# Optimization experiments

Hardware: AMD Instinct MI355X
Metric: run time of the kernel (lower is better)

Reference implementation:

```python
import jax, jax.numpy as jnp
import numpy as np

V, E, H = 50000, 256, 256   # vocab, emb_dim, hid_dim
R, S, W = 64, 32, 64        # reviews, sentences/review, words/sentence
UF = 20                     # user feature dim


def _bigru_last(x, wih, whh, bih, bhh):
    """Bidirectional GRU over x [B,T,D]; returns sum of final hidden states of
    the two directions, shape [B,H]. Params stacked over direction axis 0."""
    Hh = whh.shape[-1]

    def onedir(xd, wi, wh, bi, bh):
        gx = jnp.einsum('btd,gd->btg', xd, wi) + bi  # [B,T,3H] input gates precomputed

        def step(h, gxt):
            gh = h @ wh.T + bh
            r = jax.nn.sigmoid(gxt[:, :Hh] + gh[:, :Hh])
            z = jax.nn.sigmoid(gxt[:, Hh:2 * Hh] + gh[:, Hh:2 * Hh])
            n = jnp.tanh(gxt[:, 2 * Hh:] + r * gh[:, 2 * Hh:])
            return (1.0 - z) * n + z * h, None

        h0 = jnp.zeros((xd.shape[0], Hh), xd.dtype)
        hT, _ = jax.lax.scan(step, h0, jnp.swapaxes(gx, 0, 1))
        return hT

    return (onedir(x, wih[0], whh[0], bih[0], bhh[0])
            + onedir(x[:, ::-1], wih[1], whh[1], bih[1], bhh[1]))


def setup_inputs() -> dict:
    key = jax.random.key(0)
    ks = iter(jax.random.split(key, 40))

    def wmat(shape, scale=0.05):
        return jax.random.normal(next(ks), shape, jnp.float32) * scale

    inp = {}
    inp['inputs'] = jax.random.randint(next(ks), (R, S, W), 0, V)
    inp['sent_lengths'] = jax.random.randint(next(ks), (R, S), 1, W)
    inp['sent_counts'] = jax.random.randint(next(ks), (R,), 1, S)
    inp['user_feats'] = jax.random.normal(next(ks), (R, UF), jnp.float32)
    inp['embed'] = wmat((V, E))
    for name, din in (('wg', E), ('sg', H), ('rg', H + UF)):
        inp[name + '_wih'] = wmat((2, 3 * H, din))
        inp[name + '_whh'] = wmat((2, 3 * H, H))
        inp[name + '_bih'] = jnp.zeros((2, 3 * H), jnp.float32)
        inp[name + '_bhh'] = jnp.zeros((2, 3 * H), jnp.float32)
    inp['rfc_w1'] = wmat((H // 2, H + UF)); inp['rfc_b1'] = jnp.zeros((H // 2,), jnp.float32)
    inp['rfc_w2'] = wmat((1, H // 2));      inp['rfc_b2'] = jnp.zeros((1,), jnp.float32)
    inp['pfc_w1'] = wmat((H // 2, H));      inp['pfc_b1'] = jnp.zeros((H // 2,), jnp.float32)
    inp['pfc_w2'] = wmat((9, H // 2));      inp['pfc_b2'] = jnp.zeros((9,), jnp.float32)
    inp['uf_w'] = jnp.ones((UF,), jnp.float32)  # user_feats_weights
    return inp


def reference(inputs, sent_lengths, sent_counts, user_feats, embed,
              wg_wih, wg_whh, wg_bih, wg_bhh,
              sg_wih, sg_whh, sg_bih, sg_bhh,
              rg_wih, rg_whh, rg_bih, rg_bhh,
              rfc_w1, rfc_b1, rfc_w2, rfc_b2,
              pfc_w1, pfc_b1, pfc_w2, pfc_b2, uf_w):
    Rr, Sr, Wr = inputs.shape
    emb = embed[inputs]  # [R,S,W,E]  (dropout = identity in eval mode)
    # word-level bi-GRU, all R*S sentences batched together
    sent = _bigru_last(emb.reshape(Rr * Sr, Wr, emb.shape[-1]),
                       wg_wih, wg_whh, wg_bih, wg_bhh).reshape(Rr, Sr, -1)
    # sentence-level bi-GRU, batch over reviews
    rev = _bigru_last(sent, sg_wih, sg_whh, sg_bih, sg_bhh)  # [R,H]
    # F.normalize(user_feats) * user_feats_weights
    nrm = jnp.maximum(jnp.linalg.norm(user_feats, axis=-1, keepdims=True), 1e-12)
    p_batch = jnp.concatenate([rev, (user_feats / nrm) * uf_w], axis=-1)  # [R,H+20]
    r_stars = (jax.nn.selu(p_batch @ rfc_w1.T + rfc_b1) @ rfc_w2.T + rfc_b2)[:, 0]  # [R]
    # review-level bi-GRU over the sequence of reviews (batch 1)
    doc = _bigru_last(p_batch[None], rg_wih, rg_whh, rg_bih, rg_bhh)[0]  # [H]
    p_stars = jax.nn.selu(doc @ pfc_w1.T + pfc_b1) @ pfc_w2.T + pfc_b2  # [9]
    return p_stars, r_stars
```

## Files before the change

### kernel.cpp

```cpp
#include <hip/hip_runtime.h>
#include <math.h>

#define R_ 64
#define S_ 32
#define W_ 64
#define H_ 256
#define UF_ 20
#define TC 4

typedef short bf16x8 __attribute__((ext_vector_type(8)));
typedef float f32x4  __attribute__((ext_vector_type(4)));

#define MFMA(a,b,c) __builtin_amdgcn_mfma_f32_16x16x32_bf16((a),(b),(c),0,0,0)

typedef const unsigned int __attribute__((address_space(1)))* gp_t;
typedef unsigned int __attribute__((address_space(3)))* lp_t;
#define GLOAD16(SRC, DST) \
  __builtin_amdgcn_global_load_lds((gp_t)(const void*)(SRC), (lp_t)(void*)(DST), 16, 0, 0)

#define BFRAG(ff) ((ff) < 40 ? Breg[(ff) < 40 ? (ff) : 0] \
                 : *(const bf16x8*)&Bl[w][(ff) >= 40 ? (ff)-40 : 0][l*8])

__device__ __forceinline__ float sigf(float x){ return 1.0f/(1.0f+__expf(-x)); }
__device__ __forceinline__ float tanhf_(float x){ float e=__expf(2.0f*x); return 1.0f-2.0f/(e+1.0f); }
__device__ __forceinline__ float seluf_(float x){
  const float sc=1.0507009873554805f, al=1.6732632423543772f;
  return x>0.0f ? sc*x : sc*al*(expf(x)-1.0f);
}
__device__ __forceinline__ short tobf(float f){
  unsigned u=__float_as_uint(f); u += 0x7fffu + ((u>>16)&1u); return (short)(u>>16);
}
__device__ __forceinline__ float bf2f(short s){
  return __uint_as_float(((unsigned)(unsigned short)s) << 16);
}
__device__ __forceinline__ unsigned pk2(float a, float b){
  return (unsigned)(unsigned short)tobf(a) | ((unsigned)(unsigned short)tobf(b) << 16);
}

__global__ void prep_word_w(const float* __restrict__ wih, const float* __restrict__ whh,
                            short* __restrict__ Bw)
{
  int idx = blockIdx.x*256 + threadIdx.x;
  int lane = idx & 63;
  int rest = idx >> 6;
  int f  = rest % 6;  rest /= 6;
  int kt = rest % 16; rest /= 16;
  int w  = rest % 8;
  int d  = rest / 8;
  int gate = f >> 1;
  int j = 32*w + (f&1)*16 + (lane&15);
  int row = gate*256 + j;
  const float* W = (kt < 8 ? wih : whh) + (size_t)d*768*256;
  int k = (kt&7)*32 + (lane>>4)*8;
  short* dst = Bw + ((((size_t)(d*8 + w)*16 + kt)*6 + f)*64 + lane)*8;
#pragma unroll
  for (int jj=0;jj<8;jj++) dst[jj] = tobf(W[(size_t)row*256 + k + jj]);
}

__global__ void prep_rnn_w(const float* __restrict__ whh, short* __restrict__ Bs)
{
  int idx = blockIdx.x*256 + threadIdx.x;
  int lane = idx & 63;
  int rest = idx >> 6;
  int f  = rest % 6; rest /= 6;
  int kt = rest % 8; rest /= 8;
  int w  = rest % 8;
  int d  = rest / 8;
  int j = 32*w + (f&1)*16 + (lane&15);
  int row = (f>>1)*256 + j;
  const float* W = whh + (size_t)d*768*256;
  int k = kt*32 + (lane>>4)*8;
  short* dst = Bs + ((((size_t)(d*8 + w)*8 + kt)*6 + f)*64 + lane)*8;
#pragma unroll
  for (int jj=0;jj<8;jj++) dst[jj] = tobf(W[(size_t)row*256 + k + jj]);
}

__global__ void prep_gemm_w(const float* __restrict__ Wsrc, short* __restrict__ Bg)
{
  int idx = blockIdx.x*256 + threadIdx.x;
  int lane = idx & 63;
  int rest = idx >> 6;
  int kt = rest % 8;
  int nt = rest / 8;
  int n = nt*16 + (lane&15);
  int k = kt*32 + (lane>>4)*8;
  short* dst = Bg + (((size_t)nt*8 + kt)*64 + lane)*8;
#pragma unroll
  for (int jj=0;jj<8;jj++) dst[jj] = tobf(Wsrc[(size_t)n*256 + k + jj]);
}

__global__ __launch_bounds__(256) void gemm_gxu(
    const short* __restrict__ Ab, const float* __restrict__ Af,
    const int* __restrict__ toks, const short* __restrict__ Bg,
    short* __restrict__ C, long Czoff,
    int mode, int t0, int Mclamp, int Cstride)
{
  const int z  = blockIdx.z;
  const int m0 = blockIdx.x * 64;
  const int yt = blockIdx.y * 8;
  const int ntb = (mode == 2 ? z*48 : 0) + yt;
  const int tid = threadIdx.x;
  const int w = tid >> 6, l = tid & 63;
  const int c = l & 15, q = l >> 4;
  __shared__ short As[64][264];
  {
    const int row = tid >> 2, c0 = (tid & 3) * 64;
    if (mode == 0) {
      const uint4* s = (const uint4*)(Ab + (size_t)(m0+row)*256 + c0);
#pragma unroll
      for (int i = 0; i < 8; i++) *(uint4*)&As[row][c0 + i*8] = s[i];
    } else {
      int r;
      if (mode == 1) {
        r = m0 + row; if (r >= Mclamp) r = Mclamp - 1;
      } else {
        const int rr = m0 + row;
        const int s_ = rr / TC, i_ = rr % TC;
        const int wd = z ? (63 - (t0 + i_)) : (t0 + i_);
        r = toks[s_*64 + wd];
      }
      const float* s = Af + (size_t)r*256 + c0;
#pragma unroll
      for (int i = 0; i < 8; i++) {
        float4 v0 = *(const float4*)(s + i*8);
        float4 v1 = *(const float4*)(s + i*8 + 4);
        uint4 u;
        u.x = pk2(v0.x, v0.y); u.y = pk2(v0.z, v0.w);
        u.z = pk2(v1.x, v1.y); u.w = pk2(v1.z, v1.w);
        *(uint4*)&As[row][c0 + i*8] = u;
      }
    }
  }
  __syncthreads();
  f32x4 acc[4][2];
#pragma unroll
  for (int a = 0; a < 4; a++) { acc[a][0] = (f32x4)0.f; acc[a][1] = (f32x4)0.f; }
#pragma unroll
  for (int kt = 0; kt < 8; kt++) {
    const int ko = kt*32 + q*8;
    bf16x8 a0 = *(const bf16x8*)&As[ 0+c][ko];
    bf16x8 a1 = *(const bf16x8*)&As[16+c][ko];
    bf16x8 a2 = *(const bf16x8*)&As[32+c][ko];
    bf16x8 a3 = *(const bf16x8*)&As[48+c][ko];
    bf16x8 b0 = *(const bf16x8*)&Bg[(((size_t)(ntb + 2*w    )*8 + kt)*64 + l)*8];
    bf16x8 b1 = *(const bf16x8*)&Bg[(((size_t)(ntb + 2*w + 1)*8 + kt)*64 + l)*8];
    acc[0][0]=MFMA(a0,b0,acc[0][0]); acc[1][0]=MFMA(a1,b0,acc[1][0]);
    acc[2][0]=MFMA(a2,b0,acc[2][0]); acc[3][0]=MFMA(a3,b0,acc[3][0]);
    acc[0][1]=MFMA(a0,b1,acc[0][1]); acc[1][1]=MFMA(a1,b1,acc[1][1]);
    acc[2][1]=MFMA(a2,b1,acc[2][1]); acc[3][1]=MFMA(a3,b1,acc[3][1]);
  }
  short* Cz = C + (size_t)z * Czoff;
#pragma unroll
  for (int mt = 0; mt < 4; mt++)
#pragma unroll
  for (int nt = 0; nt < 2; nt++)
#pragma unroll
  for (int rg = 0; rg < 4; rg++)
    Cz[(size_t)(m0 + mt*16 + q*4 + rg)*Cstride + (yt + 2*w + nt)*16 + c] =
        tobf(acc[mt][nt][rg]);
}

__device__ __forceinline__ void stage_issue(
    short* dstbase,
    int mode, int d, int g, int w, int l,
    int nwords, int t0, int tt,
    const int* tokp, const short* gxF, const short* gxB)
{
  const char* bF = (const char*)gxF;
  const char* bB = (const char*)gxB;
#pragma unroll
  for (int i = 0; i < 3; i++) {
    const int off = i*1024 + l*16;
    const int rl  = (off >= 1536) ? 1 : 0;
    const int col = off - rl*1536;
    const char* src;
    if (mode == 0) {
      const int tx  = d ? (nwords - 1 - tt) : tt;
      const int tok = tokp[(2*w + rl)*64 + tx];
      src = bF + (size_t)tok*3072 + d*1536 + col;
    } else if (mode == 1) {
      const int ri = (g*16 + 2*w + rl)*TC + (tt - t0);
      src = (d ? bB : bF) + (size_t)ri*1536 + col;
    } else {
      const int se  = d ? (nwords - 1 - tt) : tt;
      const int row = g*16 + 2*w + rl;
      src = bF + ((size_t)row*nwords + se)*3072 + (size_t)d*1536 + col;
    }
    GLOAD16(src, dstbase + (size_t)w*1536 + i*512);
  }
}

__global__ __launch_bounds__(512, 2) void gru_rec(
    const int* __restrict__ toks,
    const short* __restrict__ gxF, const short* __restrict__ gxB,
    const short* __restrict__ Bh, int wstride, int koff,
    const float* __restrict__ bih, const float* __restrict__ bhh,
    float* __restrict__ hstate, int NS,
    int t0, int nsteps, int mode, int nwords)
{
  const int d = blockIdx.x & 1;
  const int g = blockIdx.x >> 1;
  const int tid = threadIdx.x;
  const int w = tid >> 6, l = tid & 63;
  const int c = l & 15, q = l >> 4;

  __shared__ short gbuf[2][16][768];
  __shared__ short hbf[2][16][264];
  __shared__ short Bl[8][8][512];
  __shared__ int   tokL[1024];

  if (mode == 0)
    for (int i = tid; i < 1024; i += 512) tokL[i] = toks[(size_t)g*1024 + i];

  bf16x8 Breg[40];
  {
    const short* Bb = Bh + (size_t)(d*8 + w)*wstride + (size_t)koff*3072 + l*8;
#pragma unroll
    for (int ff = 0; ff < 48; ff++) {
      bf16x8 v = *(const bf16x8*)(Bb + ff*512);
      if (ff < 40) Breg[ff] = v;
      else *(bf16x8*)&Bl[w][ff-40][l*8] = v;
    }
  }

  float bR[2], bZ[2], bNX[2], bNH[2];
#pragma unroll
  for (int jt = 0; jt < 2; jt++) {
    int j = 32*w + jt*16 + c;
    bR[jt]  = bih[d*768 + j]       + bhh[d*768 + j];
    bZ[jt]  = bih[d*768 + 256 + j] + bhh[d*768 + 256 + j];
    bNX[jt] = bih[d*768 + 512 + j];
    bNH[jt] = bhh[d*768 + 512 + j];
  }

  float hst[2][4];
  const int cur0 = t0 & 1;
  if (t0 == 0) {
#pragma unroll
    for (int a = 0; a < 2; a++)
#pragma unroll
    for (int r = 0; r < 4; r++) hst[a][r] = 0.0f;
  } else {
#pragma unroll
    for (int jt = 0; jt < 2; jt++)
#pragma unroll
    for (int rg = 0; rg < 4; rg++)
      hst[jt][rg] = hstate[((size_t)d*NS + g*16 + q*4 + rg)*256 + 32*w + jt*16 + c];
  }
#pragma unroll
  for (int jt = 0; jt < 2; jt++)
#pragma unroll
  for (int rg = 0; rg < 4; rg++)
    hbf[cur0][q*4 + rg][32*w + jt*16 + c] = tobf(hst[jt][rg]);

  stage_issue((short*)gbuf[cur0], mode, d, g, w, l, nwords, t0, t0,
              (mode == 0) ? toks + (size_t)g*1024 : (const int*)nullptr, gxF, gxB);

  __syncthreads();

  const int tend = t0 + nsteps;
  for (int t = t0; t < tend; t++) {
    const int cur = t & 1, nxt = 1 - cur;

    if (t + 1 < tend)
      stage_issue((short*)gbuf[nxt], mode, d, g, w, l, nwords, t0, t + 1,
                  tokL, gxF, gxB);

    f32x4 accR[2], accZ[2], accNH[2];
#pragma unroll
    for (int a = 0; a < 2; a++) { accR[a]=(f32x4)0.f; accZ[a]=(f32x4)0.f; accNH[a]=(f32x4)0.f; }
#pragma unroll
    for (int kt = 0; kt < 8; kt++) {
      bf16x8 a0 = *(const bf16x8*)&hbf[cur][c][kt*32 + q*8];
      bf16x8 b0 = BFRAG(kt*6+0), b1 = BFRAG(kt*6+1), b2 = BFRAG(kt*6+2),
             b3 = BFRAG(kt*6+3), b4 = BFRAG(kt*6+4), b5 = BFRAG(kt*6+5);
      accR[0]=MFMA(a0,b0,accR[0]);  accR[1]=MFMA(a0,b1,accR[1]);
      accZ[0]=MFMA(a0,b2,accZ[0]);  accZ[1]=MFMA(a0,b3,accZ[1]);
      accNH[0]=MFMA(a0,b4,accNH[0]); accNH[1]=MFMA(a0,b5,accNH[1]);
    }

#pragma unroll
    for (int jt = 0; jt < 2; jt++)
#pragma unroll
    for (int rg = 0; rg < 4; rg++) {
      const int m = q*4 + rg;
      const int j = 32*w + jt*16 + c;
      const float gr = bf2f(gbuf[cur][m][j]);
      const float gz = bf2f(gbuf[cur][m][256 + j]);
      const float gn = bf2f(gbuf[cur][m][512 + j]);
      const float r = sigf(gr + bR[jt] + accR[jt][rg]);
      const float z = sigf(gz + bZ[jt] + accZ[jt][rg]);
      const float n = tanhf_(gn + bNX[jt] + r*(accNH[jt][rg] + bNH[jt]));
      float h = hst[jt][rg];
      h = (1.0f - z)*n + z*h;
      hst[jt][rg] = h;
      hbf[nxt][m][j] = tobf(h);
    }
    __syncthreads();
  }

#pragma unroll
  for (int jt = 0; jt < 2; jt++)
#pragma unroll
  for (int rg = 0; rg < 4; rg++)
    hstate[((size_t)d*NS + g*16 + q*4 + rg)*256 + 32*w + jt*16 + c] = hst[jt][rg];
}

__global__ void add2bf(const float* __restrict__ a, const float* __restrict__ b,
                       short* __restrict__ o)
{
  int i = (blockIdx.x*256 + threadIdx.x)*4;
  float4 x = *(const float4*)&a[i];
  float4 y = *(const float4*)&b[i];
  *(uint2*)&o[i] = make_uint2(pk2(x.x+y.x, x.y+y.y), pk2(x.z+y.z, x.w+y.w));
}

__global__ __launch_bounds__(512, 2) void rev_gru(
    const float* __restrict__ gx, const short* __restrict__ Br,
    const float* __restrict__ bih, const float* __restrict__ bhh,
    float* __restrict__ doc)
{
  const int d = blockIdx.x;
  const int tid = threadIdx.x;
  const int w = tid >> 6, l = tid & 63;
  const int c = l & 15, q = l >> 4;

  __shared__ short hbf[2][16][264];
  __shared__ short Bl[8][8][512];
  for (int i = tid; i < 16*264; i += 512) ((short*)hbf[0])[i] = 0;

  bf16x8 Breg[40];
  {
    const short* Bbase = Br + (size_t)(d*8 + w)*8*6*512 + l*8;
#pragma unroll
    for (int ff = 0; ff < 48; ff++) {
      bf16x8 v = *(const bf16x8*)(Bbase + ff*512);
      if (ff < 40) Breg[ff] = v;
      else *(bf16x8*)&Bl[w][ff-40][l*8] = v;
    }
  }

  float bR[2], bZ[2], bNX[2], bNH[2];
#pragma unroll
  for (int jt = 0; jt < 2; jt++) {
    int j = 32*w + jt*16 + c;
    bR[jt]  = bih[d*768 + j]       + bhh[d*768 + j];
    bZ[jt]  = bih[d*768 + 256 + j] + bhh[d*768 + 256 + j];
    bNX[jt] = bih[d*768 + 512 + j];
    bNH[jt] = bhh[d*768 + 512 + j];
  }
  float hst[2][4];
#pragma unroll
  for (int a=0;a<2;a++)
#pragma unroll
  for (int r=0;r<4;r++) hst[a][r] = 0.0f;
  __syncthreads();

  for (int t = 0; t < 64; t++) {
    const int cur = t & 1, nxt = 1 - cur;
    const int teff = (d == 0) ? t : (63 - t);
    float gr[2], gz[2], gn[2];
#pragma unroll
    for (int jt = 0; jt < 2; jt++) {
      const int j = 32*w + jt*16 + c;
      const size_t row = (size_t)teff*1536 + d*768;
      gr[jt] = gx[row + j]; gz[jt] = gx[row + 256 + j]; gn[jt] = gx[row + 512 + j];
    }
    f32x4 accR[2], accZ[2], accNH[2];
#pragma unroll
    for (int a=0;a<2;a++) { accR[a]=(f32x4)0.f; accZ[a]=(f32x4)0.f; accNH[a]=(f32x4)0.f; }
#pragma unroll
    for (int kt = 0; kt < 8; kt++) {
      bf16x8 a0 = *(const bf16x8*)&hbf[cur][c][kt*32 + q*8];
      bf16x8 b0 = BFRAG(kt*6+0), b1 = BFRAG(kt*6+1), b2 = BFRAG(kt*6+2),
             b3 = BFRAG(kt*6+3), b4 = BFRAG(kt*6+4), b5 = BFRAG(kt*6+5);
      accR[0]=MFMA(a0,b0,accR[0]);  accR[1]=MFMA(a0,b1,accR[1]);
      accZ[0]=MFMA(a0,b2,accZ[0]);  accZ[1]=MFMA(a0,b3,accZ[1]);
      accNH[0]=MFMA(a0,b4,accNH[0]); accNH[1]=MFMA(a0,b5,accNH[1]);
    }
#pragma unroll
    for (int jt = 0; jt < 2; jt++)
#pragma unroll
    for (int rg = 0; rg < 4; rg++) {
      const float r = sigf(gr[jt] + bR[jt] + accR[jt][rg]);
      const float z = sigf(gz[jt] + bZ[jt] + accZ[jt][rg]);
      const float n = tanhf_(gn[jt] + bNX[jt] + r*(accNH[jt][rg] + bNH[jt]));
      float h = hst[jt][rg];
      h = (1.0f - z)*n + z*h;
      hst[jt][rg] = h;
      hbf[nxt][q*4 + rg][32*w + jt*16 + c] = tobf(h);
    }
    __syncthreads();
  }
  if (q == 0) {
#pragma unroll
    for (int jt = 0; jt < 2; jt++)
      doc[d*256 + 32*w + jt*16 + c] = hst[jt][0];
  }
}

__global__ __launch_bounds__(256) void gemm_nt16(
    const float* __restrict__ A, const float* __restrict__ B, float* __restrict__ C,
    int M, int N, int K)
{
  const int m0 = blockIdx.x * 16;
  const int n0 = blockIdx.y * 64;
  const int tid = threadIdx.x;
  __shared__ float As[16][17];
  __shared__ float Bs[16][68];
  float acc[4] = {0,0,0,0};
  const int m  = tid >> 4, n4 = (tid & 15) * 4;
  const int bn = tid >> 2, bk = (tid & 3) * 4;
  for (int k0 = 0; k0 < K; k0 += 16) {
    const int ak = tid & 15;
    float av = (k0 + ak < K) ? A[(size_t)(m0+m)*K + k0 + ak] : 0.0f;
    float4 b4 = make_float4(0,0,0,0);
    if (k0 + bk < K) b4 = *(const float4*)&B[(size_t)(n0+bn)*K + k0 + bk];
    __syncthreads();
    As[ak][m] = av;
    Bs[bk+0][bn]=b4.x; Bs[bk+1][bn]=b4.y; Bs[bk+2][bn]=b4.z; Bs[bk+3][bn]=b4.w;
    __syncthreads();
#pragma unroll
    for (int k = 0; k < 16; k++) {
      const float a = As[k][m];
      const float4 bb = *(const float4*)&Bs[k][n4];
      acc[0]+=a*bb.x; acc[1]+=a*bb.y; acc[2]+=a*bb.z; acc[3]+=a*bb.w;
    }
  }
  *(float4*)&C[(size_t)(m0+m)*N + n0+n4] = make_float4(acc[0],acc[1],acc[2],acc[3]);
}

__global__ void pbatch_k(const float* __restrict__ hs, const float* __restrict__ uf,
                         const float* __restrict__ ufw, float* __restrict__ pb)
{
  const int r = blockIdx.x, tid = threadIdx.x;
  __shared__ float nrm;
  if (tid == 0) {
    float s = 0.f;
    for (int i = 0; i < UF_; i++) { const float v = uf[r*UF_ + i]; s += v*v; }
    nrm = fmaxf(sqrtf(s), 1e-12f);
  }
  __syncthreads();
  if (tid < H_)  pb[r*276 + tid] = hs[r*H_ + tid] + hs[(size_t)R_*H_ + r*H_ + tid];
  if (tid < UF_) pb[r*276 + H_ + tid] = uf[r*UF_ + tid] / nrm * ufw[tid];
}

__global__ void rstars_k(const float* __restrict__ pb,
                         const float* __restrict__ w1, const float* __restrict__ b1,
                         const float* __restrict__ w2, const float* __restrict__ b2,
                         float* __restrict__ out)
{
  const int r = blockIdx.x, tid = threadIdx.x;
  __shared__ float ps[276];
  __shared__ float s1[128];
  for (int i = tid; i < 276; i += 128) ps[i] = pb[r*276 + i];
  __syncthreads();
  float a = b1[tid];
  for (int k = 0; k < 276; k++) a += ps[k] * w1[tid*276 + k];
  s1[tid] = seluf_(a);
  __syncthreads();
  if (tid == 0) {
    float s = b2[0];
    for (int k = 0; k < 128; k++) s += s1[k] * w2[k];
    out[9 + r] = s;
  }
}

__global__ void pstars_k(const float* __restrict__ doc2,
                         const float* __restrict__ w1, const float* __restrict__ b1,
                         const float* __restrict__ w2, const float* __restrict__ b2,
                         float* __restrict__ out)
{
  const int tid = threadIdx.x;
  __shared__ float dc[256];
  __shared__ float s1[128];
  dc[tid]       = doc2[tid]       + doc2[256 + tid];
  dc[128 + tid] = doc2[128 + tid] + doc2[384 + tid];
  __syncthreads();
  float a = b1[tid];
  for (int k = 0; k < 256; k++) a += dc[k] * w1[tid*256 + k];
  s1[tid] = seluf_(a);
  __syncthreads();
  if (tid < 9) {
    float s = b2[tid];
    for (int k = 0; k < 128; k++) s += s1[k] * w2[tid*128 + k];
    out[tid] = s;
  }
}

extern "C" void kernel_launch(void* const* d_in, const int* in_sizes, int n_in,
                              void* d_out, int out_size, void* d_ws, size_t ws_size,
                              hipStream_t stream)
{
  const int*   toks   = (const int*)  d_in[0];
  const float* uf     = (const float*)d_in[3];
  const float* embed  = (const float*)d_in[4];
  const float* wg_wih = (const float*)d_in[5];
  const float* wg_whh = (const float*)d_in[6];
  const float* wg_bih = (const float*)d_in[7];
  const float* wg_bhh = (const float*)d_in[8];
  const float* sg_wih = (const float*)d_in[9];
  const float* sg_whh = (const float*)d_in[10];
  const float* sg_bih = (const float*)d_in[11];
  const float* sg_bhh = (const float*)d_in[12];
  const float* rg_wih = (const float*)d_in[13];
  const float* rg_whh = (const float*)d_in[14];
  const float* rg_bih = (const float*)d_in[15];
  const float* rg_bhh = (const float*)d_in[16];
  const float* rfc_w1 = (const float*)d_in[17];
  const float* rfc_b1 = (const float*)d_in[18];
  const float* rfc_w2 = (const float*)d_in[19];
  const float* rfc_b2 = (const float*)d_in[20];
  const float* pfc_w1 = (const float*)d_in[21];
  const float* pfc_b1 = (const float*)d_in[22];
  const float* pfc_w2 = (const float*)d_in[23];
  const float* pfc_b2 = (const float*)d_in[24];
  const float* uf_w   = (const float*)d_in[25];
  float* out = (float*)d_out;
  float* ws  = (float*)d_ws;
  (void)in_sizes; (void)n_in; (void)out_size;

  const size_t OFF_BW   = 0;
  const size_t OFF_BS   = OFF_BW  + 393216;
  const size_t OFF_BR   = OFF_BS  + 196608;
  const size_t OFF_BG   = OFF_BR  + 196608;
  const size_t OFF_BGW  = OFF_BG  + 196608;
  const size_t OFF_HF   = OFF_BGW + 196608;
  const size_t OFF_SB   = OFF_HF  + 1048576;
  const size_t OFF_GXS  = OFF_SB  + 262144;
  const size_t OFF_HS   = OFF_GXS + 1572864;
  const size_t OFF_PB   = OFF_HS  + 32768;
  const size_t OFF_GXR  = OFF_PB  + 17664;
  const size_t OFF_DOC  = OFF_GXR + 98304;
  const size_t OFF_GXT  = OFF_DOC + 512;
  const size_t TOT_A    = OFF_GXT + (size_t)50048*1536/2;

  short* Bw   = (short*)(ws + OFF_BW);
  short* Bs   = (short*)(ws + OFF_BS);
  short* Br   = (short*)(ws + OFF_BR);
  short* Bg   = (short*)(ws + OFF_BG);
  short* Bgw  = (short*)(ws + OFF_BGW);
  float* hfin = ws + OFF_HF;
  short* sentb= (short*)(ws + OFF_SB);
  short* gxs  = (short*)(ws + OFF_GXS);
  float* hs   = ws + OFF_HS;
  float* pb   = ws + OFF_PB;
  float* gxr  = ws + OFF_GXR;
  float* doc  = ws + OFF_DOC;
  short* gxf  = (short*)(ws + OFF_GXT);
  short* gxb  = gxf + (size_t)8192*768;
  short* gxv  = (short*)(ws + OFF_GXT);

  const bool big = ws_size >= TOT_A * sizeof(float);

  prep_word_w<<<384, 256, 0, stream>>>(wg_wih, wg_whh, Bw);
  prep_rnn_w<<<192, 256, 0, stream>>>(sg_whh, Bs);
  prep_rnn_w<<<192, 256, 0, stream>>>(rg_whh, Br);
  prep_gemm_w<<<192, 256, 0, stream>>>(sg_wih, Bg);
  prep_gemm_w<<<192, 256, 0, stream>>>(wg_wih, Bgw);

  if (big) {
    gemm_gxu<<<dim3(782, 12, 1), 256, 0, stream>>>(
        nullptr, embed, nullptr, Bgw, gxv, 0, 1, 0, 50000, 1536);
    gru_rec<<<256, 512, 0, stream>>>(toks, gxv, nullptr, Bw, 49152, 8,
        wg_bih, wg_bhh, hfin, 2048, 0, 64, 0, 64);
  } else {
    for (int tc = 0; tc < 64/TC; tc++) {
      gemm_gxu<<<dim3(128, 6, 2), 256, 0, stream>>>(
          nullptr, embed, toks, Bgw, gxf, (long)8192*768, 2, tc*TC, 0, 768);
      gru_rec<<<256, 512, 0, stream>>>(toks, gxf, gxb, Bw, 49152, 8,
          wg_bih, wg_bhh, hfin, 2048, tc*TC, TC, 1, 64);
    }
  }
  add2bf<<<512, 256, 0, stream>>>(hfin, hfin + (size_t)2048*256, sentb);

  gemm_gxu<<<dim3(32, 12, 1), 256, 0, stream>>>(
      sentb, nullptr, nullptr, Bg, gxs, 0, 0, 0, 2048, 1536);
  gru_rec<<<8, 512, 0, stream>>>(nullptr, gxs, nullptr, Bs, 24576, 0,
      sg_bih, sg_bhh, hs, 64, 0, 32, 2, 32);

  pbatch_k<<<R_, 256, 0, stream>>>(hs, uf, uf_w, pb);
  rstars_k<<<R_, 128, 0, stream>>>(pb, rfc_w1, rfc_b1, rfc_w2, rfc_b2, out);

  gemm_nt16<<<dim3(4, 24), 256, 0, stream>>>(pb, rg_wih, gxr, 64, 1536, 276);
  rev_gru<<<2, 512, 0, stream>>>(gxr, Br, rg_bih, rg_bhh, doc);
  pstars_k<<<1, 128, 0, stream>>>(doc, pfc_w1, pfc_b1, pfc_w2, pfc_b2, out);
}
```

Measured before the change: 783.9 us.

## Fold GRU biases into input GEMMs and load gate inputs directly into registers

The r/z biases (bih+bhh) and the n input bias are now added in the input-projection GEMM epilogues, so the recurrent kernels only keep the hidden n bias. The async global-to-LDS double-buffered staging of gate inputs is removed. Each lane instead gathers its own gate values straight into registers every step, and the h buffer uses an XOR swizzle in place of padding to avoid LDS bank conflicts. rev_gru only updates row 0 since batch is 1, and the doc sum moves to a separate kernel. Per-step direct global gathers may expose latency that the earlier prefetch hid.

```diff
diff --git a/kernel.cpp b/kernel.cpp
--- a/kernel.cpp
+++ b/kernel.cpp
@@ -12,11 +12,6 @@
 typedef float f32x4  __attribute__((ext_vector_type(4)));
 
 #define MFMA(a,b,c) __builtin_amdgcn_mfma_f32_16x16x32_bf16((a),(b),(c),0,0,0)
-
-typedef const unsigned int __attribute__((address_space(1)))* gp_t;
-typedef unsigned int __attribute__((address_space(3)))* lp_t;
-#define GLOAD16(SRC, DST) \
-  __builtin_amdgcn_global_load_lds((gp_t)(const void*)(SRC), (lp_t)(void*)(DST), 16, 0, 0)
 
 #define BFRAG(ff) ((ff) < 40 ? Breg[(ff) < 40 ? (ff) : 0] \
                  : *(const bf16x8*)&Bl[w][(ff) >= 40 ? (ff)-40 : 0][l*8])
@@ -92,6 +87,7 @@
 __global__ __launch_bounds__(256) void gemm_gxu(
     const short* __restrict__ Ab, const float* __restrict__ Af,
     const int* __restrict__ toks, const short* __restrict__ Bg,
+    const float* __restrict__ bih, const float* __restrict__ bhh,
     short* __restrict__ C, long Czoff,
     int mode, int t0, int Mclamp, int Cstride)
 {
@@ -131,6 +127,13 @@
       }
     }
   }
+  float bias[2];
+#pragma unroll
+  for (int nt = 0; nt < 2; nt++) {
+    const int coln = (yt + 2*w + nt)*16 + c;
+    const int bidx = (mode == 2 ? z*768 : 0) + coln;
+    bias[nt] = bih[bidx] + ((bidx % 768) < 512 ? bhh[bidx] : 0.0f);
+  }
   __syncthreads();
   f32x4 acc[4][2];
 #pragma unroll
@@ -157,44 +160,14 @@
 #pragma unroll
   for (int rg = 0; rg < 4; rg++)
     Cz[(size_t)(m0 + mt*16 + q*4 + rg)*Cstride + (yt + 2*w + nt)*16 + c] =
-        tobf(acc[mt][nt][rg]);
-}
-
-__device__ __forceinline__ void stage_issue(
-    short* dstbase,
-    int mode, int d, int g, int w, int l,
-    int nwords, int t0, int tt,
-    const int* tokp, const short* gxF, const short* gxB)
-{
-  const char* bF = (const char*)gxF;
-  const char* bB = (const char*)gxB;
-#pragma unroll
-  for (int i = 0; i < 3; i++) {
-    const int off = i*1024 + l*16;
-    const int rl  = (off >= 1536) ? 1 : 0;
-    const int col = off - rl*1536;
-    const char* src;
-    if (mode == 0) {
-      const int tx  = d ? (nwords - 1 - tt) : tt;
-      const int tok = tokp[(2*w + rl)*64 + tx];
-      src = bF + (size_t)tok*3072 + d*1536 + col;
-    } else if (mode == 1) {
-      const int ri = (g*16 + 2*w + rl)*TC + (tt - t0);
-      src = (d ? bB : bF) + (size_t)ri*1536 + col;
-    } else {
-      const int se  = d ? (nwords - 1 - tt) : tt;
-      const int row = g*16 + 2*w + rl;
-      src = bF + ((size_t)row*nwords + se)*3072 + (size_t)d*1536 + col;
-    }
-    GLOAD16(src, dstbase + (size_t)w*1536 + i*512);
-  }
+        tobf(acc[mt][nt][rg] + bias[nt]);
 }
 
 __global__ __launch_bounds__(512, 2) void gru_rec(
     const int* __restrict__ toks,
     const short* __restrict__ gxF, const short* __restrict__ gxB,
     const short* __restrict__ Bh, int wstride, int koff,
-    const float* __restrict__ bih, const float* __restrict__ bhh,
+    const float* __restrict__ bhh,
     float* __restrict__ hstate, int NS,
     int t0, int nsteps, int mode, int nwords)
 {
@@ -203,9 +176,9 @@
   const int tid = threadIdx.x;
   const int w = tid >> 6, l = tid & 63;
   const int c = l & 15, q = l >> 4;
-
-  __shared__ short gbuf[2][16][768];
-  __shared__ short hbf[2][16][264];
+  const int j0 = 32*w + c;
+
+  __shared__ short hbf[2][16][256];
   __shared__ short Bl[8][8][512];
   __shared__ int   tokL[1024];
 
@@ -223,15 +196,10 @@
     }
   }
 
-  float bR[2], bZ[2], bNX[2], bNH[2];
-#pragma unroll
-  for (int jt = 0; jt < 2; jt++) {
-    int j = 32*w + jt*16 + c;
-    bR[jt]  = bih[d*768 + j]       + bhh[d*768 + j];
-    bZ[jt]  = bih[d*768 + 256 + j] + bhh[d*768 + 256 + j];
-    bNX[jt] = bih[d*768 + 512 + j];
-    bNH[jt] = bhh[d*768 + 512 + j];
-  }
+  float bNH[2];
+#pragma unroll
+  for (int jt = 0; jt < 2; jt++)
+    bNH[jt] = bhh[d*768 + 512 + j0 + jt*16];
 
   float hst[2][4];
   const int cur0 = t0 & 1;
@@ -245,16 +213,15 @@
     for (int jt = 0; jt < 2; jt++)
 #pragma unroll
     for (int rg = 0; rg < 4; rg++)
-      hst[jt][rg] = hstate[((size_t)d*NS + g*16 + q*4 + rg)*256 + 32*w + jt*16 + c];
+      hst[jt][rg] = hstate[((size_t)d*NS + g*16 + q*4 + rg)*256 + j0 + jt*16];
   }
 #pragma unroll
   for (int jt = 0; jt < 2; jt++)
 #pragma unroll
-  for (int rg = 0; rg < 4; rg++)
-    hbf[cur0][q*4 + rg][32*w + jt*16 + c] = tobf(hst[jt][rg]);
-
-  stage_issue((short*)gbuf[cur0], mode, d, g, w, l, nwords, t0, t0,
-              (mode == 0) ? toks + (size_t)g*1024 : (const int*)nullptr, gxF, gxB);
+  for (int rg = 0; rg < 4; rg++) {
+    const int m = q*4 + rg;
+    hbf[cur0][m][(j0 + jt*16) ^ ((m&7)<<3)] = tobf(hst[jt][rg]);
+  }
 
   __syncthreads();
 
@@ -262,16 +229,36 @@
   for (int t = t0; t < tend; t++) {
     const int cur = t & 1, nxt = 1 - cur;
 
-    if (t + 1 < tend)
-      stage_issue((short*)gbuf[nxt], mode, d, g, w, l, nwords, t0, t + 1,
-                  tokL, gxF, gxB);
+    const short* rb[4];
+#pragma unroll
+    for (int rg = 0; rg < 4; rg++) {
+      const int m = q*4 + rg;
+      if (mode == 0) {
+        const int tx = d ? (nwords - 1 - t) : t;
+        rb[rg] = gxF + (size_t)tokL[m*64 + tx]*1536 + d*768 + j0;
+      } else if (mode == 1) {
+        const int ri = (g*16 + m)*TC + (t - t0);
+        rb[rg] = (d ? gxB : gxF) + (size_t)ri*768 + j0;
+      } else {
+        const int se = d ? (nwords - 1 - t) : t;
+        rb[rg] = gxF + ((size_t)(g*16 + m)*nwords + se)*1536 + d*768 + j0;
+      }
+    }
+    short Gv[4][2][3];
+#pragma unroll
+    for (int rg = 0; rg < 4; rg++)
+#pragma unroll
+    for (int jt = 0; jt < 2; jt++)
+#pragma unroll
+    for (int ga = 0; ga < 3; ga++)
+      Gv[rg][jt][ga] = rb[rg][ga*256 + jt*16];
 
     f32x4 accR[2], accZ[2], accNH[2];
 #pragma unroll
     for (int a = 0; a < 2; a++) { accR[a]=(f32x4)0.f; accZ[a]=(f32x4)0.f; accNH[a]=(f32x4)0.f; }
 #pragma unroll
     for (int kt = 0; kt < 8; kt++) {
-      bf16x8 a0 = *(const bf16x8*)&hbf[cur][c][kt*32 + q*8];
+      bf16x8 a0 = *(const bf16x8*)&hbf[cur][c][(kt*32 + q*8) ^ ((c&7)<<3)];
       bf16x8 b0 = BFRAG(kt*6+0), b1 = BFRAG(kt*6+1), b2 = BFRAG(kt*6+2),
              b3 = BFRAG(kt*6+3), b4 = BFRAG(kt*6+4), b5 = BFRAG(kt*6+5);
       accR[0]=MFMA(a0,b0,accR[0]);  accR[1]=MFMA(a0,b1,accR[1]);
@@ -284,17 +271,12 @@
 #pragma unroll
     for (int rg = 0; rg < 4; rg++) {
       const int m = q*4 + rg;
-      const int j = 32*w + jt*16 + c;
-      const float gr = bf2f(gbuf[cur][m][j]);
-      const float gz = bf2f(gbuf[cur][m][256 + j]);
-      const float gn = bf2f(gbuf[cur][m][512 + j]);
-      const float r = sigf(gr + bR[jt] + accR[jt][rg]);
-      const float z = sigf(gz + bZ[jt] + accZ[jt][rg]);
-      const float n = tanhf_(gn + bNX[jt] + r*(accNH[jt][rg] + bNH[jt]));
-      float h = hst[jt][rg];
-      h = (1.0f - z)*n + z*h;
+      const float r = sigf(bf2f(Gv[rg][jt][0]) + accR[jt][rg]);
+      const float z = sigf(bf2f(Gv[rg][jt][1]) + accZ[jt][rg]);
+      const float n = tanhf_(bf2f(Gv[rg][jt][2]) + r*(accNH[jt][rg] + bNH[jt]));
+      const float h = n + z*(hst[jt][rg] - n);
       hst[jt][rg] = h;
-      hbf[nxt][m][j] = tobf(h);
+      hbf[nxt][m][(j0 + jt*16) ^ ((m&7)<<3)] = tobf(h);
     }
     __syncthreads();
   }
@@ -303,7 +285,7 @@
   for (int jt = 0; jt < 2; jt++)
 #pragma unroll
   for (int rg = 0; rg < 4; rg++)
-    hstate[((size_t)d*NS + g*16 + q*4 + rg)*256 + 32*w + jt*16 + c] = hst[jt][rg];
+    hstate[((size_t)d*NS + g*16 + q*4 + rg)*256 + j0 + jt*16] = hst[jt][rg];
 }
 
 __global__ void add2bf(const float* __restrict__ a, const float* __restrict__ b,
@@ -317,17 +299,18 @@
 
 __global__ __launch_bounds__(512, 2) void rev_gru(
     const float* __restrict__ gx, const short* __restrict__ Br,
-    const float* __restrict__ bih, const float* __restrict__ bhh,
+    const float* __restrict__ bhh,
     float* __restrict__ doc)
 {
   const int d = blockIdx.x;
   const int tid = threadIdx.x;
   const int w = tid >> 6, l = tid & 63;
   const int c = l & 15, q = l >> 4;
-
-  __shared__ short hbf[2][16][264];
+  const int j0 = 32*w + c;
+
+  __shared__ short hbf[2][16][256];
   __shared__ short Bl[8][8][512];
-  for (int i = tid; i < 16*264; i += 512) ((short*)hbf[0])[i] = 0;
+  for (int i = tid; i < 2*16*256; i += 512) ((short*)hbf)[i] = 0;
 
   bf16x8 Breg[40];
   {
@@ -340,68 +323,66 @@
     }
   }
 
-  float bR[2], bZ[2], bNX[2], bNH[2];
-#pragma unroll
-  for (int jt = 0; jt < 2; jt++) {
-    int j = 32*w + jt*16 + c;
-    bR[jt]  = bih[d*768 + j]       + bhh[d*768 + j];
-    bZ[jt]  = bih[d*768 + 256 + j] + bhh[d*768 + 256 + j];
-    bNX[jt] = bih[d*768 + 512 + j];
-    bNH[jt] = bhh[d*768 + 512 + j];
-  }
-  float hst[2][4];
-#pragma unroll
-  for (int a=0;a<2;a++)
-#pragma unroll
-  for (int r=0;r<4;r++) hst[a][r] = 0.0f;
+  float bNH[2];
+#pragma unroll
+  for (int jt = 0; jt < 2; jt++)
+    bNH[jt] = bhh[d*768 + 512 + j0 + jt*16];
+
+  float hst[2];
+  hst[0] = 0.0f; hst[1] = 0.0f;
   __syncthreads();
 
   for (int t = 0; t < 64; t++) {
     const int cur = t & 1, nxt = 1 - cur;
     const int teff = (d == 0) ? t : (63 - t);
-    float gr[2], gz[2], gn[2];
-#pragma unroll
-    for (int jt = 0; jt < 2; jt++) {
-      const int j = 32*w + jt*16 + c;
-      const size_t row = (size_t)teff*1536 + d*768;
-      gr[jt] = gx[row + j]; gz[jt] = gx[row + 256 + j]; gn[jt] = gx[row + 512 + j];
-    }
+
+    float G[2][3];
+    if (q == 0) {
+#pragma unroll
+      for (int jt = 0; jt < 2; jt++) {
+        const size_t row = (size_t)teff*1536 + d*768;
+        const int j = j0 + jt*16;
+        G[jt][0] = gx[row + j]; G[jt][1] = gx[row + 256 + j]; G[jt][2] = gx[row + 512 + j];
+      }
+    }
+
     f32x4 accR[2], accZ[2], accNH[2];
 #pragma unroll
     for (int a=0;a<2;a++) { accR[a]=(f32x4)0.f; accZ[a]=(f32x4)0.f; accNH[a]=(f32x4)0.f; }
 #pragma unroll
     for (int kt = 0; kt < 8; kt++) {
-      bf16x8 a0 = *(const bf16x8*)&hbf[cur][c][kt*32 + q*8];
+      bf16x8 a0 = *(const bf16x8*)&hbf[cur][c][(kt*32 + q*8) ^ ((c&7)<<3)];
       bf16x8 b0 = BFRAG(kt*6+0), b1 = BFRAG(kt*6+1), b2 = BFRAG(kt*6+2),
              b3 = BFRAG(kt*6+3), b4 = BFRAG(kt*6+4), b5 = BFRAG(kt*6+5);
       accR[0]=MFMA(a0,b0,accR[0]);  accR[1]=MFMA(a0,b1,accR[1]);
       accZ[0]=MFMA(a0,b2,accZ[0]);  accZ[1]=MFMA(a0,b3,accZ[1]);
       accNH[0]=MFMA(a0,b4,accNH[0]); accNH[1]=MFMA(a0,b5,accNH[1]);
     }
+
+    if (q == 0) {
+#pragma unroll
+      for (int jt = 0; jt < 2; jt++) {
+        const float r = sigf(G[jt][0] + accR[jt][0]);
+        const float z = sigf(G[jt][1] + accZ[jt][0]);
+        const float n = tanhf_(G[jt][2] + r*(accNH[jt][0] + bNH[jt]));
+        const float h = n + z*(hst[jt] - n);
+        hst[jt] = h;
+        hbf[nxt][0][j0 + jt*16] = tobf(h);
+      }
+    }
+    __syncthreads();
+  }
+  if (q == 0) {
 #pragma unroll
     for (int jt = 0; jt < 2; jt++)
-#pragma unroll
-    for (int rg = 0; rg < 4; rg++) {
-      const float r = sigf(gr[jt] + bR[jt] + accR[jt][rg]);
-      const float z = sigf(gz[jt] + bZ[jt] + accZ[jt][rg]);
-      const float n = tanhf_(gn[jt] + bNX[jt] + r*(accNH[jt][rg] + bNH[jt]));
-      float h = hst[jt][rg];
-      h = (1.0f - z)*n + z*h;
-      hst[jt][rg] = h;
-      hbf[nxt][q*4 + rg][32*w + jt*16 + c] = tobf(h);
-    }
-    __syncthreads();
-  }
-  if (q == 0) {
-#pragma unroll
-    for (int jt = 0; jt < 2; jt++)
-      doc[d*256 + 32*w + jt*16 + c] = hst[jt][0];
+      doc[d*256 + j0 + jt*16] = hst[jt];
   }
 }
 
 __global__ __launch_bounds__(256) void gemm_nt16(
-    const float* __restrict__ A, const float* __restrict__ B, float* __restrict__ C,
-    int M, int N, int K)
+    const float* __restrict__ A, const float* __restrict__ B,
+    const float* __restrict__ bih, const float* __restrict__ bhh,
+    float* __restrict__ C, int M, int N, int K)
 {
   const int m0 = blockIdx.x * 16;
   const int n0 = blockIdx.y * 64;
@@ -427,6 +408,11 @@
       acc[0]+=a*bb.x; acc[1]+=a*bb.y; acc[2]+=a*bb.z; acc[3]+=a*bb.w;
     }
   }
+#pragma unroll
+  for (int i = 0; i < 4; i++) {
+    const int n = n0 + n4 + i;
+    acc[i] += bih[n] + ((n % 768) < 512 ? bhh[n] : 0.0f);
+  }
   *(float4*)&C[(size_t)(m0+m)*N + n0+n4] = make_float4(acc[0],acc[1],acc[2],acc[3]);
 }
 
@@ -474,8 +460,8 @@
   const int tid = threadIdx.x;
   __shared__ float dc[256];
   __shared__ float s1[128];
-  dc[tid]       = doc2[tid]       + doc2[256 + tid];
-  dc[128 + tid] = doc2[128 + tid] + doc2[384 + tid];
+  dc[tid]       = doc2[tid];
+  dc[128 + tid] = doc2[128 + tid];
   __syncthreads();
   float a = b1[tid];
   for (int k = 0; k < 256; k++) a += dc[k] * w1[tid*256 + k];
@@ -486,6 +472,12 @@
     for (int k = 0; k < 128; k++) s += s1[k] * w2[tid*128 + k];
     out[tid] = s;
   }
+}
+
+__global__ void docsum_k(float* __restrict__ doc)
+{
+  const int tid = threadIdx.x;
+  doc[tid] = doc[tid] + doc[256 + tid];
 }
 
 extern "C" void kernel_launch(void* const* d_in, const int* in_sizes, int n_in,
@@ -561,28 +553,29 @@
 
   if (big) {
     gemm_gxu<<<dim3(782, 12, 1), 256, 0, stream>>>(
-        nullptr, embed, nullptr, Bgw, gxv, 0, 1, 0, 50000, 1536);
+        nullptr, embed, nullptr, Bgw, wg_bih, wg_bhh, gxv, 0, 1, 0, 50000, 1536);
     gru_rec<<<256, 512, 0, stream>>>(toks, gxv, nullptr, Bw, 49152, 8,
-        wg_bih, wg_bhh, hfin, 2048, 0, 64, 0, 64);
+        wg_bhh, hfin, 2048, 0, 64, 0, 64);
   } else {
     for (int tc = 0; tc < 64/TC; tc++) {
       gemm_gxu<<<dim3(128, 6, 2), 256, 0, stream>>>(
-          nullptr, embed, toks, Bgw, gxf, (long)8192*768, 2, tc*TC, 0, 768);
+          nullptr, embed, toks, Bgw, wg_bih, wg_bhh, gxf, (long)8192*768, 2, tc*TC, 0, 768);
       gru_rec<<<256, 512, 0, stream>>>(toks, gxf, gxb, Bw, 49152, 8,
-          wg_bih, wg_bhh, hfin, 2048, tc*TC, TC, 1, 64);
+          wg_bhh, hfin, 2048, tc*TC, TC, 1, 64);
     }
   }
   add2bf<<<512, 256, 0, stream>>>(hfin, hfin + (size_t)2048*256, sentb);
 
   gemm_gxu<<<dim3(32, 12, 1), 256, 0, stream>>>(
-      sentb, nullptr, nullptr, Bg, gxs, 0, 0, 0, 2048, 1536);
+      sentb, nullptr, nullptr, Bg, sg_bih, sg_bhh, gxs, 0, 0, 0, 2048, 1536);
   gru_rec<<<8, 512, 0, stream>>>(nullptr, gxs, nullptr, Bs, 24576, 0,
-      sg_bih, sg_bhh, hs, 64, 0, 32, 2, 32);
+      sg_bhh, hs, 64, 0, 32, 2, 32);
 
   pbatch_k<<<R_, 256, 0, stream>>>(hs, uf, uf_w, pb);
   rstars_k<<<R_, 128, 0, stream>>>(pb, rfc_w1, rfc_b1, rfc_w2, rfc_b2, out);
 
-  gemm_nt16<<<dim3(4, 24), 256, 0, stream>>>(pb, rg_wih, gxr, 64, 1536, 276);
-  rev_gru<<<2, 512, 0, stream>>>(gxr, Br, rg_bih, rg_bhh, doc);
+  gemm_nt16<<<dim3(4, 24), 256, 0, stream>>>(pb, rg_wih, rg_bih, rg_bhh, gxr, 64, 1536, 276);
+  rev_gru<<<2, 512, 0, stream>>>(gxr, Br, rg_bhh, doc);
+  docsum_k<<<1, 256, 0, stream>>>(doc);
   pstars_k<<<1, 128, 0, stream>>>(doc, pfc_w1, pfc_b1, pfc_w2, pfc_b2, out);
 }
```

After: 805.1 us. 2.7% more time.
